# Optimization experiments

Hardware: AMD Instinct MI355X
Metric: run time of the kernel (lower is better)

The kernel has to match this reference:

```python
import jax, jax.numpy as jnp
import numpy as np

BN_EPS = 1e-5

def setup_inputs() -> dict:
    key = jax.random.key(0)
    k1, k2, k3 = jax.random.split(key, 3)
    B, N, C, K, O = 4, 16384, 64, 16, 64
    x = jax.random.normal(k1, (B, N, C), dtype=jnp.float32)
    idx = jax.random.randint(k2, (B, N, K), 0, N, dtype=jnp.int32)
    weight = jax.random.normal(k3, (O, 2 * C), dtype=jnp.float32) * 0.05
    gamma = jnp.ones((O,), dtype=jnp.float32)
    beta = jnp.zeros((O,), dtype=jnp.float32)
    return {"x": x, "idx": idx, "weight": weight, "gamma": gamma, "beta": beta}

def reference(x, idx, weight, gamma, beta):
    # x: [B,N,C], idx: [B,N,k] kNN indices into N
    B, N, C = x.shape
    k = idx.shape[2]
    # irregular gather: neighbor features [B,N,k,C]
    batch_ix = jnp.arange(B)[:, None, None]
    neighbor = x[batch_ix, idx]                     # [B,N,k,C]
    center = x[:, :, None, :]                       # [B,N,1,C]
    diff = neighbor - center                        # [B,N,k,C]
    edge = jnp.concatenate([jnp.broadcast_to(center, (B, N, k, C)), diff], axis=-1)  # [B,N,k,2C]
    # 1x1 conv == per-edge linear transform: [B,N,k,O]
    h = jnp.einsum('bnkc,oc->bnko', edge, weight)
    # BatchNorm2d in training mode: stats over (B,N,k) per output channel
    mean = jnp.mean(h, axis=(0, 1, 2))
    var = jnp.var(h, axis=(0, 1, 2))
    h = (h - mean) * jax.lax.rsqrt(var + BN_EPS) * gamma + beta
    h = jax.nn.relu(h)
    # max-pool over k neighbors -> [B,N,O]
    out = jnp.max(h, axis=2)
    return out
```

## Files before the change

kernel.cpp:

```cpp
#include <hip/hip_runtime.h>
#include <math.h>

#define BN_EPS 1e-5f

constexpr int B_ = 4, N_ = 16384, C_ = 64, K_ = 16, O_ = 64;
constexpr int ROWS = B_ * N_;
constexpr int ROWS_PER_BLK = 64;
constexpr int NBLK_AB = ROWS / ROWS_PER_BLK;

__device__ __forceinline__ float b2f(unsigned short u) {
    return __uint_as_float(((unsigned)u) << 16);
}
__device__ __forceinline__ unsigned short f2b(float f) {
    unsigned u = __float_as_uint(f);
    return (unsigned short)((u + 0x7fffu + ((u >> 16) & 1u)) >> 16);
}

__global__ __launch_bounds__(256) void pass_a(const float* __restrict__ x,
                                              const float* __restrict__ w,
                                              float* __restrict__ y1,
                                              unsigned short* __restrict__ y2) {
    __shared__ float w1m[64 * 65];
    __shared__ float w2s[64 * 65];
    __shared__ float xs[64 * 64];
    const int tid = threadIdx.x;

    for (int i = tid; i < 64 * 64; i += 256) {
        int o = i >> 6, c = i & 63;
        float a = w[o * 128 + c];
        float b = w[o * 128 + 64 + c];
        w1m[c * 65 + o] = a - b;
        w2s[c * 65 + o] = b;
    }
    const long base = (long)blockIdx.x * ROWS_PER_BLK;
    const float* xsrc = x + base * 64;
    for (int i = tid; i < 64 * 64; i += 256) xs[i] = xsrc[i];
    __syncthreads();

    const int o  = tid & 63;
    const int rr = tid >> 6;
    for (int chunk = 0; chunk < 4; ++chunk) {
        const int r0 = chunk * 16 + rr * 4;
        float a1[4] = {0.f, 0.f, 0.f, 0.f};
        float a2[4] = {0.f, 0.f, 0.f, 0.f};
        for (int c4 = 0; c4 < 16; ++c4) {
            float4 xv[4];
#pragma unroll
            for (int j = 0; j < 4; ++j)
                xv[j] = *(const float4*)&xs[(r0 + j) * 64 + c4 * 4];
#pragma unroll
            for (int cc = 0; cc < 4; ++cc) {
                const int c = c4 * 4 + cc;
                const float wv1 = w1m[c * 65 + o];
                const float wv2 = w2s[c * 65 + o];
                const float xj0 = (&xv[0].x)[cc], xj1 = (&xv[1].x)[cc];
                const float xj2 = (&xv[2].x)[cc], xj3 = (&xv[3].x)[cc];
                a1[0] = fmaf(xj0, wv1, a1[0]); a2[0] = fmaf(xj0, wv2, a2[0]);
                a1[1] = fmaf(xj1, wv1, a1[1]); a2[1] = fmaf(xj1, wv2, a2[1]);
                a1[2] = fmaf(xj2, wv1, a1[2]); a2[2] = fmaf(xj2, wv2, a2[2]);
                a1[3] = fmaf(xj3, wv1, a1[3]); a2[3] = fmaf(xj3, wv2, a2[3]);
            }
        }
#pragma unroll
        for (int j = 0; j < 4; ++j) {
            y1[(base + r0 + j) * 64 + o] = a1[j];
            y2[(base + r0 + j) * 64 + o] = f2b(a2[j]);
        }
    }
}

__global__ __launch_bounds__(256) void pass_b(const float* __restrict__ y1,
                                              const unsigned short* __restrict__ y2,
                                              const int* __restrict__ idx,
                                              const float* __restrict__ gamma,
                                              unsigned short* __restrict__ exth,
                                              float* __restrict__ partial) {
    __shared__ int sidx[ROWS_PER_BLK * K_];
    __shared__ float reds[4][64];
    __shared__ float redq[4][64];
    const int tid = threadIdx.x;
    const int blk = blockIdx.x;
    const int xcd = blk & 7;
    const int bt = xcd >> 1;
    const int slot = ((blk >> 3) << 1) | (xcd & 1);
    const long base = (long)bt * N_ + (long)slot * ROWS_PER_BLK;

    ((int4*)sidx)[tid] = ((const int4*)(idx + base * K_))[tid];

    const int lane = tid & 63;
    const int wv   = tid >> 6;
    const int ksub = lane >> 4;
    const int c4   = lane & 15;
    const unsigned short* y2b = y2 + (long)bt * N_ * 64;

    const float4 gm = ((const float4*)gamma)[c4];
    const float4 sgn = make_float4(gm.x >= 0.f ? 1.f : -1.f,
                                   gm.y >= 0.f ? 1.f : -1.f,
                                   gm.z >= 0.f ? 1.f : -1.f,
                                   gm.w >= 0.f ? 1.f : -1.f);
    __syncthreads();

    float4 psum = make_float4(0.f, 0.f, 0.f, 0.f);
    float4 psq  = make_float4(0.f, 0.f, 0.f, 0.f);

    for (int rl = wv; rl < ROWS_PER_BLK; rl += 4) {
        const long row = base + rl;
        const float4 y1v = ((const float4*)(y1 + row * 64))[c4];
        float4 e = make_float4(-3.402823466e+38f, -3.402823466e+38f,
                               -3.402823466e+38f, -3.402823466e+38f);
#pragma unroll
        for (int kk = 0; kk < 4; ++kk) {
            const int m = sidx[rl * K_ + kk * 4 + ksub];
            const ushort4 v = *(const ushort4*)(y2b + (long)m * 64 + c4 * 4);
            const float hx = y1v.x + b2f(v.x), hy = y1v.y + b2f(v.y);
            const float hz = y1v.z + b2f(v.z), hw = y1v.w + b2f(v.w);
            e.x = fmaxf(e.x, sgn.x * hx); e.y = fmaxf(e.y, sgn.y * hy);
            e.z = fmaxf(e.z, sgn.z * hz); e.w = fmaxf(e.w, sgn.w * hw);
            psum.x += hx; psum.y += hy; psum.z += hz; psum.w += hw;
            psq.x = fmaf(hx, hx, psq.x); psq.y = fmaf(hy, hy, psq.y);
            psq.z = fmaf(hz, hz, psq.z); psq.w = fmaf(hw, hw, psq.w);
        }
#pragma unroll
        for (int d = 16; d <= 32; d <<= 1) {
            e.x = fmaxf(e.x, __shfl_xor(e.x, d));
            e.y = fmaxf(e.y, __shfl_xor(e.y, d));
            e.z = fmaxf(e.z, __shfl_xor(e.z, d));
            e.w = fmaxf(e.w, __shfl_xor(e.w, d));
        }
        if (ksub == 0) {
            ushort4 r;
            r.x = f2b(sgn.x * e.x); r.y = f2b(sgn.y * e.y);
            r.z = f2b(sgn.z * e.z); r.w = f2b(sgn.w * e.w);
            *(ushort4*)(exth + row * 64 + c4 * 4) = r;
        }
    }
#pragma unroll
    for (int d = 16; d <= 32; d <<= 1) {
        psum.x += __shfl_xor(psum.x, d); psum.y += __shfl_xor(psum.y, d);
        psum.z += __shfl_xor(psum.z, d); psum.w += __shfl_xor(psum.w, d);
        psq.x  += __shfl_xor(psq.x, d);  psq.y  += __shfl_xor(psq.y, d);
        psq.z  += __shfl_xor(psq.z, d);  psq.w  += __shfl_xor(psq.w, d);
    }
    if (ksub == 0) {
        *(float4*)&reds[wv][c4 * 4] = psum;
        *(float4*)&redq[wv][c4 * 4] = psq;
    }
    __syncthreads();
    if (tid < 64) {
        const float s = reds[0][tid] + reds[1][tid] + reds[2][tid] + reds[3][tid];
        const float q = redq[0][tid] + redq[1][tid] + redq[2][tid] + redq[3][tid];
        partial[blk * 128 + tid] = s;
        partial[blk * 128 + 64 + tid] = q;
    }
}

__global__ __launch_bounds__(256) void pass_c(const float* __restrict__ partial,
                                              const float* __restrict__ gamma,
                                              const float* __restrict__ beta,
                                              float* __restrict__ ss) {
    __shared__ double rs[256];
    __shared__ double rq[256];
    const int o = blockIdx.x;
    const int tid = threadIdx.x;
    double as = 0.0, aq = 0.0;
    for (int i = tid; i < NBLK_AB; i += 256) {
        as += (double)partial[i * 128 + o];
        aq += (double)partial[i * 128 + 64 + o];
    }
    rs[tid] = as;
    rq[tid] = aq;
    __syncthreads();
    for (int s = 128; s > 0; s >>= 1) {
        if (tid < s) { rs[tid] += rs[tid + s]; rq[tid] += rq[tid + s]; }
        __syncthreads();
    }
    if (tid == 0) {
        const double cnt = (double)B_ * N_ * K_;
        double mean = rs[0] / cnt;
        double var = rq[0] / cnt - mean * mean;
        float scale = gamma[o] * (float)(1.0 / sqrt(var + (double)BN_EPS));
        float shift = beta[o] - (float)mean * scale;
        ss[o] = scale;
        ss[64 + o] = shift;
    }
}

__global__ __launch_bounds__(256) void pass_d(const unsigned short* __restrict__ exth,
                                              const float* __restrict__ ss,
                                              float* __restrict__ out) {
    __shared__ float sscale[64], sshift[64];
    const int tid = threadIdx.x;
    if (tid < 64) { sscale[tid] = ss[tid]; sshift[tid] = ss[64 + tid]; }
    __syncthreads();
    const uint4* ep = (const uint4*)exth;
    const long total8 = (long)ROWS * 64 / 8;
    for (long i = (long)blockIdx.x * 256 + tid; i < total8;
         i += (long)gridDim.x * 256) {
        const int c0 = ((int)i * 8) & 63;
        const uint4 u = ep[i];
        const unsigned uu[4] = {u.x, u.y, u.z, u.w};
        float r[8];
#pragma unroll
        for (int j = 0; j < 4; ++j) {
            const float e0 = __uint_as_float(uu[j] << 16);
            const float e1 = __uint_as_float(uu[j] & 0xffff0000u);
            r[2 * j]     = fmaxf(fmaf(sscale[c0 + 2 * j],     e0, sshift[c0 + 2 * j]),     0.f);
            r[2 * j + 1] = fmaxf(fmaf(sscale[c0 + 2 * j + 1], e1, sshift[c0 + 2 * j + 1]), 0.f);
        }
        ((float4*)out)[2 * i]     = make_float4(r[0], r[1], r[2], r[3]);
        ((float4*)out)[2 * i + 1] = make_float4(r[4], r[5], r[6], r[7]);
    }
}

extern "C" void kernel_launch(void* const* d_in, const int* in_sizes, int n_in,
                              void* d_out, int out_size, void* d_ws, size_t ws_size,
                              hipStream_t stream) {
    const float* x     = (const float*)d_in[0];
    const int*   idx   = (const int*)d_in[1];
    const float* w     = (const float*)d_in[2];
    const float* gamma = (const float*)d_in[3];
    const float* beta  = (const float*)d_in[4];
    float* out = (float*)d_out;

    char* ws = (char*)d_ws;
    float*          y1      = (float*)ws;
    unsigned short* y2      = (unsigned short*)(ws + 16777216);
    unsigned short* exth    = (unsigned short*)(ws + 25165824);
    float*          partial = (float*)(ws + 33554432);
    float*          ss      = (float*)(ws + 34078720);

    pass_a<<<NBLK_AB, 256, 0, stream>>>(x, w, y1, y2);
    pass_b<<<NBLK_AB, 256, 0, stream>>>(y1, y2, idx, gamma, exth, partial);
    pass_c<<<64, 256, 0, stream>>>(partial, gamma, beta, ss);
    pass_d<<<2048, 256, 0, stream>>>(exth, ss, out);
}
```

Measured before the change: 126.0 us.

## Fuse gather, BN-stat reduction and normalize into one cooperative kernel

Merges the gather/max pass, the per-channel statistics reduction and the final normalize/ReLU pass into a single cooperative kernel separated by two grid-wide syncs. Per-row max values now stay in shared memory as fp32 instead of a bf16 round trip through global memory. This removes two kernel launches and the intermediate exth buffer traffic. In exchange, all 1024 blocks must be co-resident, and the reduction phase runs on only 64 blocks while the rest wait at the grid barrier.

```diff
diff --git a/kernel.cpp b/kernel.cpp
--- a/kernel.cpp
+++ b/kernel.cpp
@@ -1,12 +1,15 @@
 #include <hip/hip_runtime.h>
+#include <hip/hip_cooperative_groups.h>
 #include <math.h>
+
+namespace cg = cooperative_groups;
 
 #define BN_EPS 1e-5f
 
 constexpr int B_ = 4, N_ = 16384, C_ = 64, K_ = 16, O_ = 64;
 constexpr int ROWS = B_ * N_;
 constexpr int ROWS_PER_BLK = 64;
-constexpr int NBLK_AB = ROWS / ROWS_PER_BLK;
+constexpr int NBLK = ROWS / ROWS_PER_BLK;
 
 __device__ __forceinline__ float b2f(unsigned short u) {
     return __uint_as_float(((unsigned)u) << 16);
@@ -69,15 +72,22 @@
     }
 }
 
-__global__ __launch_bounds__(256) void pass_b(const float* __restrict__ y1,
-                                              const unsigned short* __restrict__ y2,
-                                              const int* __restrict__ idx,
-                                              const float* __restrict__ gamma,
-                                              unsigned short* __restrict__ exth,
-                                              float* __restrict__ partial) {
+__global__ __launch_bounds__(256, 4) void pass_bcd(
+        const float* __restrict__ y1,
+        const unsigned short* __restrict__ y2,
+        const int* __restrict__ idx,
+        const float* __restrict__ gamma,
+        const float* __restrict__ beta,
+        float* __restrict__ partial,
+        float* __restrict__ ss,
+        float* __restrict__ out) {
     __shared__ int sidx[ROWS_PER_BLK * K_];
+    __shared__ float eL[64 * 64];
     __shared__ float reds[4][64];
     __shared__ float redq[4][64];
+    __shared__ double rs[256];
+    __shared__ double rq[256];
+
     const int tid = threadIdx.x;
     const int blk = blockIdx.x;
     const int xcd = blk & 7;
@@ -127,12 +137,8 @@
             e.z = fmaxf(e.z, __shfl_xor(e.z, d));
             e.w = fmaxf(e.w, __shfl_xor(e.w, d));
         }
-        if (ksub == 0) {
-            ushort4 r;
-            r.x = f2b(sgn.x * e.x); r.y = f2b(sgn.y * e.y);
-            r.z = f2b(sgn.z * e.z); r.w = f2b(sgn.w * e.w);
-            *(ushort4*)(exth + row * 64 + c4 * 4) = r;
-        }
+        if (ksub == 0)
+            *(float4*)&eL[rl * 64 + c4 * 4] = e;
     }
 #pragma unroll
     for (int d = 16; d <= 32; d <<= 1) {
@@ -152,63 +158,53 @@
         partial[blk * 128 + tid] = s;
         partial[blk * 128 + 64 + tid] = q;
     }
-}
-
-__global__ __launch_bounds__(256) void pass_c(const float* __restrict__ partial,
-                                              const float* __restrict__ gamma,
-                                              const float* __restrict__ beta,
-                                              float* __restrict__ ss) {
-    __shared__ double rs[256];
-    __shared__ double rq[256];
-    const int o = blockIdx.x;
-    const int tid = threadIdx.x;
-    double as = 0.0, aq = 0.0;
-    for (int i = tid; i < NBLK_AB; i += 256) {
-        as += (double)partial[i * 128 + o];
-        aq += (double)partial[i * 128 + 64 + o];
-    }
-    rs[tid] = as;
-    rq[tid] = aq;
-    __syncthreads();
-    for (int s = 128; s > 0; s >>= 1) {
-        if (tid < s) { rs[tid] += rs[tid + s]; rq[tid] += rq[tid + s]; }
+    __threadfence();
+
+    cg::this_grid().sync();
+
+    if (blk < 64) {
+        const int o = blk;
+        double as = 0.0, aq = 0.0;
+        for (int i = tid; i < NBLK; i += 256) {
+            as += (double)partial[i * 128 + o];
+            aq += (double)partial[i * 128 + 64 + o];
+        }
+        rs[tid] = as;
+        rq[tid] = aq;
         __syncthreads();
-    }
-    if (tid == 0) {
-        const double cnt = (double)B_ * N_ * K_;
-        double mean = rs[0] / cnt;
-        double var = rq[0] / cnt - mean * mean;
-        float scale = gamma[o] * (float)(1.0 / sqrt(var + (double)BN_EPS));
-        float shift = beta[o] - (float)mean * scale;
-        ss[o] = scale;
-        ss[64 + o] = shift;
-    }
-}
-
-__global__ __launch_bounds__(256) void pass_d(const unsigned short* __restrict__ exth,
-                                              const float* __restrict__ ss,
-                                              float* __restrict__ out) {
-    __shared__ float sscale[64], sshift[64];
-    const int tid = threadIdx.x;
-    if (tid < 64) { sscale[tid] = ss[tid]; sshift[tid] = ss[64 + tid]; }
-    __syncthreads();
-    const uint4* ep = (const uint4*)exth;
-    const long total8 = (long)ROWS * 64 / 8;
-    for (long i = (long)blockIdx.x * 256 + tid; i < total8;
-         i += (long)gridDim.x * 256) {
-        const int c0 = ((int)i * 8) & 63;
-        const uint4 u = ep[i];
-        const unsigned uu[4] = {u.x, u.y, u.z, u.w};
-        float r[8];
-#pragma unroll
-        for (int j = 0; j < 4; ++j) {
-            const float e0 = __uint_as_float(uu[j] << 16);
-            const float e1 = __uint_as_float(uu[j] & 0xffff0000u);
-            r[2 * j]     = fmaxf(fmaf(sscale[c0 + 2 * j],     e0, sshift[c0 + 2 * j]),     0.f);
-            r[2 * j + 1] = fmaxf(fmaf(sscale[c0 + 2 * j + 1], e1, sshift[c0 + 2 * j + 1]), 0.f);
-        }
-        ((float4*)out)[2 * i]     = make_float4(r[0], r[1], r[2], r[3]);
-        ((float4*)out)[2 * i + 1] = make_float4(r[4], r[5], r[6], r[7]);
+        for (int s = 128; s > 0; s >>= 1) {
+            if (tid < s) { rs[tid] += rs[tid + s]; rq[tid] += rq[tid + s]; }
+            __syncthreads();
+        }
+        if (tid == 0) {
+            const double cnt = (double)B_ * N_ * K_;
+            double mean = rs[0] / cnt;
+            double var = rq[0] / cnt - mean * mean;
+            float scale = gamma[o] * (float)(1.0 / sqrt(var + (double)BN_EPS));
+            float shift = beta[o] - (float)mean * scale;
+            ss[o] = scale;
+            ss[64 + o] = shift;
+        }
+        __threadfence();
+    }
+
+    cg::this_grid().sync();
+
+    if (tid < 64) {
+        reds[0][tid] = fabsf(ss[tid]);
+        reds[1][tid] = ss[64 + tid];
+    }
+    __syncthreads();
+    for (int i = tid; i < 1024; i += 256) {
+        const int row = i >> 4;
+        const int c0 = (i & 15) * 4;
+        const float4 e4 = *(const float4*)&eL[row * 64 + c0];
+        float4 r;
+        r.x = fmaxf(fmaf(reds[0][c0],     e4.x, reds[1][c0]),     0.f);
+        r.y = fmaxf(fmaf(reds[0][c0 + 1], e4.y, reds[1][c0 + 1]), 0.f);
+        r.z = fmaxf(fmaf(reds[0][c0 + 2], e4.z, reds[1][c0 + 2]), 0.f);
+        r.w = fmaxf(fmaf(reds[0][c0 + 3], e4.w, reds[1][c0 + 3]), 0.f);
+        *(float4*)&out[(base + row) * 64 + c0] = r;
     }
 }
 
@@ -225,12 +221,13 @@
     char* ws = (char*)d_ws;
     float*          y1      = (float*)ws;
     unsigned short* y2      = (unsigned short*)(ws + 16777216);
-    unsigned short* exth    = (unsigned short*)(ws + 25165824);
-    float*          partial = (float*)(ws + 33554432);
-    float*          ss      = (float*)(ws + 34078720);
-
-    pass_a<<<NBLK_AB, 256, 0, stream>>>(x, w, y1, y2);
-    pass_b<<<NBLK_AB, 256, 0, stream>>>(y1, y2, idx, gamma, exth, partial);
-    pass_c<<<64, 256, 0, stream>>>(partial, gamma, beta, ss);
-    pass_d<<<2048, 256, 0, stream>>>(exth, ss, out);
-}
+    float*          partial = (float*)(ws + 25165824);
+    float*          ss      = (float*)(ws + 25690112);
+
+    pass_a<<<NBLK, 256, 0, stream>>>(x, w, y1, y2);
+
+    void* args[] = {(void*)&y1, (void*)&y2, (void*)&idx, (void*)&gamma,
+                    (void*)&beta, (void*)&partial, (void*)&ss, (void*)&out};
+    hipLaunchCooperativeKernel((const void*)pass_bcd, dim3(NBLK), dim3(256),
+                               args, 0, stream);
+}
```

Result: slower. 372.2 us (+195.3%).
